# Optimization experiments

Hardware: AMD Instinct MI355X
Metric: run time of the kernel (lower is better)

Reference implementation:

```python
import jax, jax.numpy as jnp
import numpy as np

NUM_HEADS = 16
ROPE_BASE = 10000.0


def _rope(x):
    # x: (B, T, H, D); torchtune-style interleaved rotary embedding
    B, T, H, D = x.shape
    inv_freq = 1.0 / (ROPE_BASE ** (jnp.arange(0, D, 2, dtype=jnp.float32) / D))  # (D/2,)
    ang = jnp.arange(T, dtype=jnp.float32)[:, None] * inv_freq[None, :]  # (T, D/2)
    cos = jnp.cos(ang)[None, :, None, :].astype(x.dtype)  # (1,T,1,D/2)
    sin = jnp.sin(ang)[None, :, None, :].astype(x.dtype)
    x1 = x[..., 0::2]
    x2 = x[..., 1::2]
    r1 = x1 * cos - x2 * sin
    r2 = x2 * cos + x1 * sin
    return jnp.stack([r1, r2], axis=-1).reshape(B, T, H, D)


def _attention(x, Wq, Wk, Wv, Wo, bo):
    B, T, C = x.shape
    H = NUM_HEADS
    D = C // H
    q = (x @ Wq).reshape(B, T, H, D)
    k = (x @ Wk).reshape(B, T, H, D)
    v = (x @ Wv).reshape(B, T, H, D)
    q = _rope(q)
    k = _rope(k)
    # (B, H, T, D)
    q = q.transpose(0, 2, 1, 3)
    k = k.transpose(0, 2, 1, 3)
    v = v.transpose(0, 2, 1, 3)
    scale = 1.0 / jnp.sqrt(jnp.asarray(D, dtype=x.dtype))
    scores = jnp.einsum('bhqd,bhkd->bhqk', q, k) * scale  # (B,H,T,T)
    causal = jnp.tril(jnp.ones((T, T), dtype=bool))
    scores = jnp.where(causal[None, None, :, :], scores, jnp.asarray(-jnp.inf, dtype=scores.dtype))
    attn = jax.nn.softmax(scores, axis=-1)
    out = jnp.einsum('bhqk,bhkd->bhqd', attn, v)  # (B,H,T,D)
    out = out.transpose(0, 2, 1, 3).reshape(B, T, C)
    return out @ Wo + bo  # dropout is identity in eval mode


def setup_inputs() -> dict:
    key = jax.random.key(0)
    ks = jax.random.split(key, 6)
    B, T, C = 2, 2048, 1024
    s = 1.0 / np.sqrt(C)
    return {
        'x': jax.random.normal(ks[0], (B, T, C), dtype=jnp.float32),
        'Wq': jax.random.normal(ks[1], (C, C), dtype=jnp.float32) * s,
        'Wk': jax.random.normal(ks[2], (C, C), dtype=jnp.float32) * s,
        'Wv': jax.random.normal(ks[3], (C, C), dtype=jnp.float32) * s,
        'Wo': jax.random.normal(ks[4], (C, C), dtype=jnp.float32) * s,
        'bo': jnp.zeros((C,), dtype=jnp.float32),
    }


def reference(x, Wq, Wk, Wv, Wo, bo):
    return _attention(x, Wq, Wk, Wv, Wo, bo)
```

## Files before the change

### kernel.cpp

```cpp
#include <hip/hip_runtime.h>
#include <stdint.h>

#define BATCH 2
#define T_SEQ 2048
#define CDIM  1024
#define NH    16
#define HD    64
#define MROWS (BATCH*T_SEQ)

typedef unsigned short u16;
typedef __attribute__((ext_vector_type(8))) short bf16x8;
typedef __attribute__((ext_vector_type(4))) float f32x4;
typedef __attribute__((ext_vector_type(16))) float f32x16;
typedef __attribute__((ext_vector_type(4))) unsigned short u16x4;

__constant__ int qc_tab[40] = {0,1,2,3, 4,4,5,5,6,6,7,7,
                               8,8,8,9,9,9,10,10,10,11,11,11,
                               12,12,12,12,13,13,13,13,14,14,14,14,15,15,15,15};
__constant__ int ck_tab[40] = {0,0,0,0, 0,1,0,1,0,1,0,1,
                               0,1,2,0,1,2,0,1,2,0,1,2,
                               0,1,2,3,0,1,2,3,0,1,2,3,0,1,2,3};
__constant__ int base_tab[16] = {0,1,2,3,4,6,8,10,12,15,18,21,24,28,32,36};
__constant__ int nch_tab[16]  = {1,1,1,1,2,2,2,2,3,3,3,3,4,4,4,4};

__device__ __forceinline__ u16 f2b(float f) {
  union { float f; unsigned int u; } x; x.f = f;
  unsigned int r = x.u + 0x7FFFu + ((x.u >> 16) & 1u);
  return (u16)(r >> 16);
}

__device__ __forceinline__ void gload16(const void* g, void* s) {
  __builtin_amdgcn_global_load_lds(
      (const __attribute__((address_space(1))) void*)g,
      (__attribute__((address_space(3))) void*)s, 16, 0, 0);
}

__device__ __forceinline__ int cvtpk(float lo, float hi_) {
  int w;
  asm("v_cvt_pk_bf16_f32 %0, %1, %2" : "=v"(w) : "v"(lo), "v"(hi_));
  return w;
}

__device__ __forceinline__ bf16x8 mkfrag(int a, int b, int c, int d) {
  union { int i[4]; bf16x8 v; } u;
  u.i[0] = a; u.i[1] = b; u.i[2] = c; u.i[3] = d;
  return u.v;
}

__global__ __launch_bounds__(256) void cvt4(const float4* __restrict__ in,
                                            u16x4* __restrict__ out, int n4) {
  int i = blockIdx.x * 256 + threadIdx.x;
  if (i < n4) {
    float4 v = in[i];
    u16x4 o = { f2b(v.x), f2b(v.y), f2b(v.z), f2b(v.w) };
    out[i] = o;
  }
}

__global__ __launch_bounds__(256) void w_trans4(const float* __restrict__ W0,
                                                const float* __restrict__ W1,
                                                const float* __restrict__ W2,
                                                const float* __restrict__ W3,
                                                u16* __restrict__ D0,
                                                u16* __restrict__ D3) {
  __shared__ u16 tile[64][72];
  const float* W = (blockIdx.z == 0) ? W0 : (blockIdx.z == 1) ? W1
                 : (blockIdx.z == 2) ? W2 : W3;
  u16* Wt = (blockIdx.z == 3) ? D3 : (D0 + (size_t)blockIdx.z * CDIM * CDIM);
  int k0 = blockIdx.x * 64, n0 = blockIdx.y * 64;
  int tid = threadIdx.x;
  #pragma unroll
  for (int i = 0; i < 16; ++i) {
    int c = i * 256 + tid;
    int kr = c >> 6, nc = c & 63;
    tile[kr][nc] = f2b(W[(size_t)(k0 + kr) * CDIM + n0 + nc]);
  }
  __syncthreads();
  #pragma unroll
  for (int i = 0; i < 16; ++i) {
    int c = i * 256 + tid;
    int nr = c >> 6, kc = c & 63;
    Wt[(size_t)(n0 + nr) * CDIM + k0 + kc] = tile[kc][nr];
  }
}

__global__ __launch_bounds__(256) void rope_tab(float* __restrict__ cosT,
                                                float* __restrict__ sinT) {
  int i = blockIdx.x * 256 + threadIdx.x;
  int t = i >> 5, j = i & 31;
  float inv = expf(-(float)j * (9.210340371976184f / 32.0f));
  float ang = (float)t * inv;
  cosT[i] = cosf(ang);
  sinT[i] = sinf(ang);
}

__global__ __launch_bounds__(512, 2) void gemm_qkv256(const u16* __restrict__ A,
                                                      const u16* __restrict__ Bt,
                                                      const float* __restrict__ cosT,
                                                      const float* __restrict__ sinT,
                                                      u16* __restrict__ Qr,
                                                      u16* __restrict__ Kr,
                                                      u16* __restrict__ Vt) {
  __shared__ __align__(16) char smem[114688];
  const int tid = threadIdx.x;
  const int wid = tid >> 6, lane = tid & 63;
  const int wm = wid >> 2, wn = wid & 3;
  const int col = lane & 15, kq = lane >> 4;
  const int xcd = blockIdx.x & 7, bi = blockIdx.x >> 3;
  const int arow0 = (bi & 15) * 256;
  const int bcol0 = (xcd * 2 + (bi >> 4)) * 192;

  auto STAGE = [&](int k0, int bsel) {
    char* dA = smem + bsel * 57344;
    char* dB = dA + 32768;
    #pragma unroll
    for (int i = 0; i < 4; ++i) {
      int idx = i * 512 + tid;
      int r = idx >> 3, p = idx & 7;
      int src = (p ^ (r & 7)) << 3;
      gload16(A + (size_t)(arow0 + r) * CDIM + k0 + src, dA + idx * 16);
    }
    #pragma unroll
    for (int i = 0; i < 3; ++i) {
      int idx = i * 512 + tid;
      int r = idx >> 3, p = idx & 7;
      int src = (p ^ (r & 7)) << 3;
      gload16(Bt + (size_t)(bcol0 + r) * CDIM + k0 + src, dB + idx * 16);
    }
  };

  f32x4 acc[8][3] = {};

  STAGE(0, 0);
  for (int kt = 0; kt < 16; ++kt) {
    if (kt < 15) {
      STAGE((kt + 1) * 64, (kt + 1) & 1);
      asm volatile("s_waitcnt vmcnt(7)" ::: "memory");
    } else {
      asm volatile("s_waitcnt vmcnt(0)" ::: "memory");
    }
    __builtin_amdgcn_s_barrier();

    const char* As_ = smem + (kt & 1) * 57344;
    const char* Bs_ = As_ + 32768;

    bf16x8 bfr[3][2], a0[4][2], a1[4][2];
    #pragma unroll
    for (int n = 0; n < 3; ++n)
      #pragma unroll
      for (int ks = 0; ks < 2; ++ks) {
        int rowb = wn * 48 + n * 16 + col;
        bfr[n][ks] = *(const bf16x8*)(Bs_ + rowb * 128 + (((ks * 4 + kq) ^ (rowb & 7)) << 4));
      }
    #pragma unroll
    for (int m = 0; m < 4; ++m)
      #pragma unroll
      for (int ks = 0; ks < 2; ++ks) {
        int row = wm * 128 + m * 16 + col;
        a0[m][ks] = *(const bf16x8*)(As_ + row * 128 + (((ks * 4 + kq) ^ (row & 7)) << 4));
        int row1 = row + 64;
        a1[m][ks] = *(const bf16x8*)(As_ + row1 * 128 + (((ks * 4 + kq) ^ (row1 & 7)) << 4));
      }

    __builtin_amdgcn_s_setprio(1);
    #pragma unroll
    for (int m = 0; m < 4; ++m)
      #pragma unroll
      for (int n = 0; n < 3; ++n)
        #pragma unroll
        for (int ks = 0; ks < 2; ++ks)
          acc[m][n] = __builtin_amdgcn_mfma_f32_16x16x32_bf16(a0[m][ks], bfr[n][ks],
                                                              acc[m][n], 0, 0, 0);
    #pragma unroll
    for (int m = 0; m < 4; ++m)
      #pragma unroll
      for (int n = 0; n < 3; ++n)
        #pragma unroll
        for (int ks = 0; ks < 2; ++ks)
          acc[4 + m][n] = __builtin_amdgcn_mfma_f32_16x16x32_bf16(a1[m][ks], bfr[n][ks],
                                                                  acc[4 + m][n], 0, 0, 0);
    __builtin_amdgcn_s_setprio(0);
    __builtin_amdgcn_s_barrier();
  }

  #pragma unroll
  for (int im = 0; im < 8; ++im)
    #pragma unroll
    for (int in = 0; in < 3; ++in) {
      int cc = bcol0 + wn * 48 + in * 16 + col;
      int type = cc >> 10;
      int cm = cc & 1023;
      int h = cm >> 6, d = cm & 63;
      int rr0 = arow0 + wm * 128 + im * 16 + kq * 4;
      if (type == 2) {
        int b = rr0 >> 11, t = rr0 & 2047;
        u16x4 v4 = { f2b(acc[im][in][0]), f2b(acc[im][in][1]),
                     f2b(acc[im][in][2]), f2b(acc[im][in][3]) };
        *(u16x4*)(Vt + (((size_t)(b * NH + h)) * 64 + d) * T_SEQ + t) = v4;
      } else {
        int j = d >> 1;
        u16* dst = type ? Kr : Qr;
        #pragma unroll
        for (int i = 0; i < 4; ++i) {
          int rr = rr0 + i;
          int b = rr >> 11, t = rr & 2047;
          float val = acc[im][in][i];
          float pv = __shfl_xor(val, 1, 64);
          float c = cosT[t * 32 + j], s = sinT[t * 32 + j];
          float r = (d & 1) ? (val * c + pv * s) : (val * c - pv * s);
          if (type == 0) r *= 0.18033688011112042f;
          dst[(((size_t)(b * NH + h)) * T_SEQ + t) * 64 + d] = f2b(r);
        }
      }
    }
}

__global__ __launch_bounds__(256, 2) void gemm_bt(const u16* __restrict__ A,
                                                  const u16* __restrict__ Bt,
                                                  float* __restrict__ C,
                                                  const float* __restrict__ bias,
                                                  int K, int ldc) {
  __shared__ __align__(16) char smem[65536];
  const int tid = threadIdx.x;
  const int wid = tid >> 6, lane = tid & 63;
  const int wr = wid >> 1, wc = wid & 1;
  const int col = lane & 15, kq = lane >> 4;
  const int swz = (blockIdx.x & 7) * 32 + (blockIdx.x >> 3);
  const int arow0 = (swz & 31) * 128, bcol0 = (swz >> 5) * 128;
  const int NT = K >> 6;

  auto STAGE = [&](int k0, int bsel) {
    char* dA = smem + bsel * 32768;
    char* dB = dA + 16384;
    #pragma unroll
    for (int i = 0; i < 4; ++i) {
      int idx = i * 256 + tid;
      int r = idx >> 3, p = idx & 7;
      int src = (p ^ (r & 7)) << 3;
      gload16(A  + (size_t)(arow0 + r) * K + k0 + src, dA + idx * 16);
      gload16(Bt + (size_t)(bcol0 + r) * K + k0 + src, dB + idx * 16);
    }
  };

  f32x4 acc[4][4] = {};

  STAGE(0, 0);
  for (int kt = 0; kt < NT; ++kt) {
    if (kt + 1 < NT) {
      STAGE((kt + 1) * 64, (kt + 1) & 1);
      asm volatile("s_waitcnt vmcnt(8)" ::: "memory");
    } else {
      asm volatile("s_waitcnt vmcnt(0)" ::: "memory");
    }
    __builtin_amdgcn_s_barrier();
    const char* As_ = smem + (kt & 1) * 32768;
    const char* Bs_ = As_ + 16384;
    bf16x8 a[4][2], b[4][2];
    #pragma unroll
    for (int m = 0; m < 4; ++m)
      #pragma unroll
      for (int ks = 0; ks < 2; ++ks) {
        int row = wr * 64 + m * 16 + col;
        a[m][ks] = *(const bf16x8*)(As_ + row * 128 + (((ks * 4 + kq) ^ (row & 7)) << 4));
      }
    #pragma unroll
    for (int n = 0; n < 4; ++n)
      #pragma unroll
      for (int ks = 0; ks < 2; ++ks) {
        int rowb = wc * 64 + n * 16 + col;
        b[n][ks] = *(const bf16x8*)(Bs_ + rowb * 128 + (((ks * 4 + kq) ^ (rowb & 7)) << 4));
      }
    __builtin_amdgcn_s_setprio(1);
    #pragma unroll
    for (int m = 0; m < 4; ++m)
      #pragma unroll
      for (int n = 0; n < 4; ++n)
        #pragma unroll
        for (int ks = 0; ks < 2; ++ks)
          acc[m][n] = __builtin_amdgcn_mfma_f32_16x16x32_bf16(a[m][ks], b[n][ks],
                                                              acc[m][n], 0, 0, 0);
    __builtin_amdgcn_s_setprio(0);
    __builtin_amdgcn_s_barrier();
  }

  #pragma unroll
  for (int m = 0; m < 4; ++m)
    #pragma unroll
    for (int n = 0; n < 4; ++n) {
      int cc = bcol0 + wc * 64 + n * 16 + col;
      float bv = bias ? bias[cc] : 0.0f;
      #pragma unroll
      for (int i = 0; i < 4; ++i) {
        int rr = arow0 + wr * 64 + m * 16 + kq * 4 + i;
        C[(size_t)rr * ldc + cc] = acc[m][n][i] + bv;
      }
    }
}

__global__ __launch_bounds__(256, 4) void attn_fwd8(const u16* __restrict__ Q,
                                                    const u16* __restrict__ K,
                                                    const u16* __restrict__ V,
                                                    float* __restrict__ OP,
                                                    float* __restrict__ LP) {
  __shared__ __align__(16) char smem[32768];

  const int bh = blockIdx.x;
  const int w = 39 - blockIdx.y;
  const int qc = qc_tab[w], ck = ck_tab[w];
  const int q0 = qc << 7;
  const int nkt = 2 * (qc + 1);
  const int start = ck * 8;
  const int end = min(start + 8, nkt);
  const int slot = w * 32 + bh;

  const int tid = threadIdx.x;
  const int wid = tid >> 6, lane = tid & 63;
  const int l31 = lane & 31, hi = lane >> 5;
  const int wq0 = q0 + wid * 32;
  const int qrow = wq0 + l31;

  bf16x8 qa[4];
  const u16* qbase = Q + ((size_t)bh * T_SEQ + qrow) * 64 + hi * 8;
  #pragma unroll
  for (int dk = 0; dk < 4; ++dk)
    qa[dk] = *(const bf16x8*)(qbase + dk * 16);

  const u16* kb = K + (size_t)bh * T_SEQ * 64;
  const u16* vb = V + (size_t)bh * 64 * T_SEQ;

  auto STAGE = [&](int kt, int bsel) {
    char* dstK = smem + bsel * 16384;
    char* dstV = dstK + 8192;
    int kv0 = kt << 6;
    #pragma unroll
    for (int i = 0; i < 2; ++i) {
      int idx = i * 256 + tid;
      int r = idx >> 3, c = idx & 7;
      int cs = (c ^ (r & 7)) << 3;
      gload16(kb + (size_t)(kv0 + r) * 64 + cs, dstK + idx * 16);
      gload16(vb + (size_t)r * T_SEQ + kv0 + cs, dstV + idx * 16);
    }
  };

  float L = 0.f;
  f32x16 ot0 = {}, ot1 = {};
  const int swl = (l31 & 7);

  STAGE(start, 0);

  for (int kt = start; kt < end; ++kt) {
    const int kv0 = kt << 6;
    const int cur = (kt - start) & 1;
    if (kt + 1 < end) {
      STAGE(kt + 1, cur ^ 1);
      asm volatile("s_waitcnt vmcnt(4)" ::: "memory");
    } else {
      asm volatile("s_waitcnt vmcnt(0)" ::: "memory");
    }
    __builtin_amdgcn_s_barrier();

    if (kv0 <= wq0 + 31) {
      const char* Ks = smem + cur * 16384;
      const char* Vs = Ks + 8192;

      f32x16 st0 = {}, st1 = {};
      __builtin_amdgcn_s_setprio(1);
      #pragma unroll
      for (int dk = 0; dk < 4; ++dk) {
        int ch = dk * 2 + hi;
        bf16x8 ka0 = *(const bf16x8*)(Ks + l31 * 128 + ((ch ^ swl) << 4));
        bf16x8 ka1 = *(const bf16x8*)(Ks + (l31 + 32) * 128 + ((ch ^ swl) << 4));
        st0 = __builtin_amdgcn_mfma_f32_32x32x16_bf16(ka0, qa[dk], st0, 0, 0, 0);
        st1 = __builtin_amdgcn_mfma_f32_32x32x16_bf16(ka1, qa[dk], st1, 0, 0, 0);
      }
      __builtin_amdgcn_s_setprio(0);

      if (kv0 + 63 > wq0) {
        #pragma unroll
        for (int r = 0; r < 16; ++r) {
          int kl = (r & 3) + 8 * (r >> 2) + 4 * hi;
          if (kv0 + kl > qrow)      st0[r] = -1e30f;
          if (kv0 + 32 + kl > qrow) st1[r] = -1e30f;
        }
      }

      float s0 = 0.f, s1 = 0.f, s2 = 0.f, s3 = 0.f;
      #pragma unroll
      for (int r = 0; r < 16; r += 4) {
        st0[r]     = exp2f(st0[r]     - 14.f); st1[r]     = exp2f(st1[r]     - 14.f);
        st0[r + 1] = exp2f(st0[r + 1] - 14.f); st1[r + 1] = exp2f(st1[r + 1] - 14.f);
        st0[r + 2] = exp2f(st0[r + 2] - 14.f); st1[r + 2] = exp2f(st1[r + 2] - 14.f);
        st0[r + 3] = exp2f(st0[r + 3] - 14.f); st1[r + 3] = exp2f(st1[r + 3] - 14.f);
        s0 += st0[r]     + st1[r];
        s1 += st0[r + 1] + st1[r + 1];
        s2 += st0[r + 2] + st1[r + 2];
        s3 += st0[r + 3] + st1[r + 3];
      }
      float sum = (s0 + s1) + (s2 + s3);
      sum += __shfl_xor(sum, 32, 64);
      L += sum;

      int x0 = cvtpk(st0[0], st0[1]),   y0 = cvtpk(st0[4], st0[5]);
      int x1 = cvtpk(st0[2], st0[3]),   y1 = cvtpk(st0[6], st0[7]);
      int x2 = cvtpk(st0[8], st0[9]),   y2 = cvtpk(st0[12], st0[13]);
      int x3 = cvtpk(st0[10], st0[11]), y3 = cvtpk(st0[14], st0[15]);
      asm("v_permlane32_swap_b32 %0, %1" : "+v"(x0), "+v"(y0));
      asm("v_permlane32_swap_b32 %0, %1" : "+v"(x1), "+v"(y1));
      asm("v_permlane32_swap_b32 %0, %1" : "+v"(x2), "+v"(y2));
      asm("v_permlane32_swap_b32 %0, %1" : "+v"(x3), "+v"(y3));
      int z0 = cvtpk(st1[0], st1[1]),   w0 = cvtpk(st1[4], st1[5]);
      int z1 = cvtpk(st1[2], st1[3]),   w1 = cvtpk(st1[6], st1[7]);
      int z2 = cvtpk(st1[8], st1[9]),   w2 = cvtpk(st1[12], st1[13]);
      int z3 = cvtpk(st1[10], st1[11]), w3 = cvtpk(st1[14], st1[15]);
      asm("v_permlane32_swap_b32 %0, %1" : "+v"(z0), "+v"(w0));
      asm("v_permlane32_swap_b32 %0, %1" : "+v"(z1), "+v"(w1));
      asm("v_permlane32_swap_b32 %0, %1" : "+v"(z2), "+v"(w2));
      asm("v_permlane32_swap_b32 %0, %1" : "+v"(z3), "+v"(w3));
      bf16x8 pb[4];
      pb[0] = mkfrag(x0, x1, y0, y1);
      pb[1] = mkfrag(x2, x3, y2, y3);
      pb[2] = mkfrag(z0, z1, w0, w1);
      pb[3] = mkfrag(z2, z3, w2, w3);

      __builtin_amdgcn_s_setprio(1);
      #pragma unroll
      for (int ks = 0; ks < 4; ++ks) {
        int ch = ks * 2 + hi;
        bf16x8 va0 = *(const bf16x8*)(Vs + l31 * 128 + ((ch ^ swl) << 4));
        bf16x8 va1 = *(const bf16x8*)(Vs + (l31 + 32) * 128 + ((ch ^ swl) << 4));
        ot0 = __builtin_amdgcn_mfma_f32_32x32x16_bf16(va0, pb[ks], ot0, 0, 0, 0);
        ot1 = __builtin_amdgcn_mfma_f32_32x32x16_bf16(va1, pb[ks], ot1, 0, 0, 0);
      }
      __builtin_amdgcn_s_setprio(0);
    }

    asm volatile("s_waitcnt lgkmcnt(0)" ::: "memory");
    __builtin_amdgcn_s_barrier();
  }

  float* op = OP + (size_t)slot * 8192;
  const int qloc = wid * 32 + l31;
  #pragma unroll
  for (int r = 0; r < 16; ++r) {
    int d_ = (r & 3) + 8 * (r >> 2) + 4 * hi;
    op[d_ * 128 + qloc]        = ot0[r];
    op[(32 + d_) * 128 + qloc] = ot1[r];
  }
  if (hi == 0) LP[(size_t)slot * 128 + qloc] = L;
}

__global__ __launch_bounds__(256) void attn_comb(const float* __restrict__ OP,
                                                 const float* __restrict__ LP,
                                                 u16* __restrict__ Ob) {
  __shared__ float tr[64 * 132];
  const int qc = blockIdx.x, head = blockIdx.y;
  const int nch = nch_tab[qc], base = base_tab[qc];
  const int tid = threadIdx.x;

  {
    int d = tid >> 2, q4 = (tid & 3) * 32;
    float a[32];
    #pragma unroll
    for (int j = 0; j < 32; ++j) a[j] = 0.f;
    for (int c = 0; c < nch; ++c) {
      const float* p = OP + ((size_t)((base + c) * 32 + head)) * 8192 + d * 128 + q4;
      #pragma unroll
      for (int j = 0; j < 8; ++j) {
        float4 v = *(const float4*)(p + j * 4);
        a[j * 4]     += v.x; a[j * 4 + 1] += v.y;
        a[j * 4 + 2] += v.z; a[j * 4 + 3] += v.w;
      }
    }
    #pragma unroll
    for (int j = 0; j < 32; ++j) tr[d * 132 + q4 + j] = a[j];
  }
  __syncthreads();

  int q = tid >> 1, d0 = (tid & 1) * 32;
  float Lt = 0.f;
  for (int c = 0; c < nch; ++c)
    Lt += LP[((size_t)((base + c) * 32 + head)) * 128 + q];
  float inv = 1.0f / Lt;

  int outw[16];
  #pragma unroll
  for (int j = 0; j < 16; ++j) {
    float lo  = tr[(d0 + 2 * j) * 132 + q] * inv;
    float hi_ = tr[(d0 + 2 * j + 1) * 132 + q] * inv;
    outw[j] = cvtpk(lo, hi_);
  }
  int b = head >> 4, h = head & 15;
  size_t row = (size_t)(b * T_SEQ + qc * 128 + q);
  int* dst = (int*)(Ob + row * 1024 + h * 64 + d0);
  #pragma unroll
  for (int j = 0; j < 4; ++j) {
    int4 v = { outw[j * 4], outw[j * 4 + 1], outw[j * 4 + 2], outw[j * 4 + 3] };
    *(int4*)(dst + j * 4) = v;
  }
}

extern "C" void kernel_launch(void* const* d_in, const int* in_sizes, int n_in,
                              void* d_out, int out_size, void* d_ws, size_t ws_size,
                              hipStream_t stream) {
  (void)in_sizes; (void)n_in; (void)out_size; (void)ws_size;
  const float* x  = (const float*)d_in[0];
  const float* Wq = (const float*)d_in[1];
  const float* Wk = (const float*)d_in[2];
  const float* Wv = (const float*)d_in[3];
  const float* Wo = (const float*)d_in[4];
  const float* bo = (const float*)d_in[5];
  float* out = (float*)d_out;

  char* ws = (char*)d_ws;
  u16*   xb   = (u16*)(ws);
  u16*   Wqkv = (u16*)(ws + (size_t)( 8u << 20));
  u16*   Wot  = (u16*)(ws + (size_t)(14u << 20));
  u16*   Qr   = (u16*)(ws + (size_t)(16u << 20));
  u16*   Kr   = (u16*)(ws + (size_t)(24u << 20));
  u16*   Vt   = (u16*)(ws + (size_t)(32u << 20));
  u16*   Ob   = (u16*)(ws + (size_t)(40u << 20));
  float* cosT = (float*)(ws + (size_t)(48u << 20));
  float* sinT = (float*)(ws + (size_t)(48u << 20) + (1u << 18));
  float* OP   = (float*)(ws + (size_t)(49u << 20));
  float* LP   = (float*)(ws + (size_t)(89u << 20));

  cvt4<<<dim3(MROWS * CDIM / 4 / 256), dim3(256), 0, stream>>>(
      (const float4*)x, (u16x4*)xb, MROWS * CDIM / 4);
  w_trans4<<<dim3(16, 16, 4), dim3(256), 0, stream>>>(Wq, Wk, Wv, Wo, Wqkv, Wot);
  rope_tab<<<dim3(T_SEQ * 32 / 256), dim3(256), 0, stream>>>(cosT, sinT);

  gemm_qkv256<<<dim3(256), dim3(512), 0, stream>>>(xb, Wqkv, cosT, sinT, Qr, Kr, Vt);

  attn_fwd8<<<dim3(32, 40), dim3(256), 0, stream>>>(Qr, Kr, Vt, OP, LP);
  attn_comb<<<dim3(16, 32), dim3(256), 0, stream>>>(OP, LP, Ob);

  gemm_bt<<<dim3(256), dim3(256), 0, stream>>>(Ob, Wot, out, bo, CDIM, CDIM);
}
```

Before: 116.4 us.

## Give each attention wave two 32-row query tiles, halving block size

The flash-attention kernel now runs 2 waves per block instead of 4, and each wave handles 64 query rows as two 32-row sub-tiles that share the same K and V fragments loaded from LDS. Staging loops are widened so 128 threads still fill the same K/V tiles, and the wait counts are adjusted to match. The aim is to cut LDS reads per MFMA and barrier overhead. The cost is more VGPRs (twice the accumulators) and lower occupancy, plus coarser causal skipping per wave.

```diff
diff --git a/kernel.cpp b/kernel.cpp
--- a/kernel.cpp
+++ b/kernel.cpp
@@ -297,7 +297,7 @@
     }
 }
 
-__global__ __launch_bounds__(256, 4) void attn_fwd8(const u16* __restrict__ Q,
+__global__ __launch_bounds__(128, 2) void attn_fwd9(const u16* __restrict__ Q,
                                                     const u16* __restrict__ K,
                                                     const u16* __restrict__ V,
                                                     float* __restrict__ OP,
@@ -316,14 +316,17 @@
   const int tid = threadIdx.x;
   const int wid = tid >> 6, lane = tid & 63;
   const int l31 = lane & 31, hi = lane >> 5;
-  const int wq0 = q0 + wid * 32;
-  const int qrow = wq0 + l31;
-
-  bf16x8 qa[4];
-  const u16* qbase = Q + ((size_t)bh * T_SEQ + qrow) * 64 + hi * 8;
-  #pragma unroll
-  for (int dk = 0; dk < 4; ++dk)
-    qa[dk] = *(const bf16x8*)(qbase + dk * 16);
+  const int wq0 = q0 + wid * 64;
+  const int qrowA = wq0 + l31;
+  const int qrowB = wq0 + 32 + l31;
+
+  bf16x8 qaA[4], qaB[4];
+  const u16* qbA = Q + ((size_t)bh * T_SEQ + qrowA) * 64 + hi * 8;
+  #pragma unroll
+  for (int dk = 0; dk < 4; ++dk) {
+    qaA[dk] = *(const bf16x8*)(qbA + dk * 16);
+    qaB[dk] = *(const bf16x8*)(qbA + 2048 + dk * 16);
+  }
 
   const u16* kb = K + (size_t)bh * T_SEQ * 64;
   const u16* vb = V + (size_t)bh * 64 * T_SEQ;
@@ -333,8 +336,8 @@
     char* dstV = dstK + 8192;
     int kv0 = kt << 6;
     #pragma unroll
-    for (int i = 0; i < 2; ++i) {
-      int idx = i * 256 + tid;
+    for (int i = 0; i < 4; ++i) {
+      int idx = i * 128 + tid;
       int r = idx >> 3, c = idx & 7;
       int cs = (c ^ (r & 7)) << 3;
       gload16(kb + (size_t)(kv0 + r) * 64 + cs, dstK + idx * 16);
@@ -342,8 +345,8 @@
     }
   };
 
-  float L = 0.f;
-  f32x16 ot0 = {}, ot1 = {};
+  float LA = 0.f, LB = 0.f;
+  f32x16 oA0 = {}, oA1 = {}, oB0 = {}, oB1 = {};
   const int swl = (l31 & 7);
 
   STAGE(start, 0);
@@ -353,25 +356,27 @@
     const int cur = (kt - start) & 1;
     if (kt + 1 < end) {
       STAGE(kt + 1, cur ^ 1);
-      asm volatile("s_waitcnt vmcnt(4)" ::: "memory");
+      asm volatile("s_waitcnt vmcnt(8)" ::: "memory");
     } else {
       asm volatile("s_waitcnt vmcnt(0)" ::: "memory");
     }
     __builtin_amdgcn_s_barrier();
 
-    if (kv0 <= wq0 + 31) {
+    if (kv0 <= wq0 + 63) {
       const char* Ks = smem + cur * 16384;
       const char* Vs = Ks + 8192;
 
-      f32x16 st0 = {}, st1 = {};
+      f32x16 sA0 = {}, sA1 = {}, sB0 = {}, sB1 = {};
       __builtin_amdgcn_s_setprio(1);
       #pragma unroll
       for (int dk = 0; dk < 4; ++dk) {
         int ch = dk * 2 + hi;
         bf16x8 ka0 = *(const bf16x8*)(Ks + l31 * 128 + ((ch ^ swl) << 4));
         bf16x8 ka1 = *(const bf16x8*)(Ks + (l31 + 32) * 128 + ((ch ^ swl) << 4));
-        st0 = __builtin_amdgcn_mfma_f32_32x32x16_bf16(ka0, qa[dk], st0, 0, 0, 0);
-        st1 = __builtin_amdgcn_mfma_f32_32x32x16_bf16(ka1, qa[dk], st1, 0, 0, 0);
+        sA0 = __builtin_amdgcn_mfma_f32_32x32x16_bf16(ka0, qaA[dk], sA0, 0, 0, 0);
+        sA1 = __builtin_amdgcn_mfma_f32_32x32x16_bf16(ka1, qaA[dk], sA1, 0, 0, 0);
+        sB0 = __builtin_amdgcn_mfma_f32_32x32x16_bf16(ka0, qaB[dk], sB0, 0, 0, 0);
+        sB1 = __builtin_amdgcn_mfma_f32_32x32x16_bf16(ka1, qaB[dk], sB1, 0, 0, 0);
       }
       __builtin_amdgcn_s_setprio(0);
 
@@ -379,48 +384,78 @@
         #pragma unroll
         for (int r = 0; r < 16; ++r) {
           int kl = (r & 3) + 8 * (r >> 2) + 4 * hi;
-          if (kv0 + kl > qrow)      st0[r] = -1e30f;
-          if (kv0 + 32 + kl > qrow) st1[r] = -1e30f;
+          if (kv0 + kl > qrowA)      sA0[r] = -1e30f;
+          if (kv0 + 32 + kl > qrowA) sA1[r] = -1e30f;
         }
       }
-
-      float s0 = 0.f, s1 = 0.f, s2 = 0.f, s3 = 0.f;
-      #pragma unroll
-      for (int r = 0; r < 16; r += 4) {
-        st0[r]     = exp2f(st0[r]     - 14.f); st1[r]     = exp2f(st1[r]     - 14.f);
-        st0[r + 1] = exp2f(st0[r + 1] - 14.f); st1[r + 1] = exp2f(st1[r + 1] - 14.f);
-        st0[r + 2] = exp2f(st0[r + 2] - 14.f); st1[r + 2] = exp2f(st1[r + 2] - 14.f);
-        st0[r + 3] = exp2f(st0[r + 3] - 14.f); st1[r + 3] = exp2f(st1[r + 3] - 14.f);
-        s0 += st0[r]     + st1[r];
-        s1 += st0[r + 1] + st1[r + 1];
-        s2 += st0[r + 2] + st1[r + 2];
-        s3 += st0[r + 3] + st1[r + 3];
-      }
-      float sum = (s0 + s1) + (s2 + s3);
-      sum += __shfl_xor(sum, 32, 64);
-      L += sum;
-
-      int x0 = cvtpk(st0[0], st0[1]),   y0 = cvtpk(st0[4], st0[5]);
-      int x1 = cvtpk(st0[2], st0[3]),   y1 = cvtpk(st0[6], st0[7]);
-      int x2 = cvtpk(st0[8], st0[9]),   y2 = cvtpk(st0[12], st0[13]);
-      int x3 = cvtpk(st0[10], st0[11]), y3 = cvtpk(st0[14], st0[15]);
+      if (kv0 + 63 > wq0 + 32) {
+        #pragma unroll
+        for (int r = 0; r < 16; ++r) {
+          int kl = (r & 3) + 8 * (r >> 2) + 4 * hi;
+          if (kv0 + kl > qrowB)      sB0[r] = -1e30f;
+          if (kv0 + 32 + kl > qrowB) sB1[r] = -1e30f;
+        }
+      }
+
+      float a0_ = 0.f, a1_ = 0.f, b0_ = 0.f, b1_ = 0.f;
+      #pragma unroll
+      for (int r = 0; r < 16; r += 2) {
+        sA0[r]     = exp2f(sA0[r]     - 14.f); sA1[r]     = exp2f(sA1[r]     - 14.f);
+        sA0[r + 1] = exp2f(sA0[r + 1] - 14.f); sA1[r + 1] = exp2f(sA1[r + 1] - 14.f);
+        sB0[r]     = exp2f(sB0[r]     - 14.f); sB1[r]     = exp2f(sB1[r]     - 14.f);
+        sB0[r + 1] = exp2f(sB0[r + 1] - 14.f); sB1[r + 1] = exp2f(sB1[r + 1] - 14.f);
+        a0_ += sA0[r] + sA1[r];  a1_ += sA0[r + 1] + sA1[r + 1];
+        b0_ += sB0[r] + sB1[r];  b1_ += sB0[r + 1] + sB1[r + 1];
+      }
+      float sa = a0_ + a1_, sb = b0_ + b1_;
+      sa += __shfl_xor(sa, 32, 64);
+      sb += __shfl_xor(sb, 32, 64);
+      LA += sa;
+      LB += sb;
+
+      int x0 = cvtpk(sA0[0], sA0[1]),   y0 = cvtpk(sA0[4], sA0[5]);
+      int x1 = cvtpk(sA0[2], sA0[3]),   y1 = cvtpk(sA0[6], sA0[7]);
+      int x2 = cvtpk(sA0[8], sA0[9]),   y2 = cvtpk(sA0[12], sA0[13]);
+      int x3 = cvtpk(sA0[10], sA0[11]), y3 = cvtpk(sA0[14], sA0[15]);
       asm("v_permlane32_swap_b32 %0, %1" : "+v"(x0), "+v"(y0));
       asm("v_permlane32_swap_b32 %0, %1" : "+v"(x1), "+v"(y1));
       asm("v_permlane32_swap_b32 %0, %1" : "+v"(x2), "+v"(y2));
       asm("v_permlane32_swap_b32 %0, %1" : "+v"(x3), "+v"(y3));
-      int z0 = cvtpk(st1[0], st1[1]),   w0 = cvtpk(st1[4], st1[5]);
-      int z1 = cvtpk(st1[2], st1[3]),   w1 = cvtpk(st1[6], st1[7]);
-      int z2 = cvtpk(st1[8], st1[9]),   w2 = cvtpk(st1[12], st1[13]);
-      int z3 = cvtpk(st1[10], st1[11]), w3 = cvtpk(st1[14], st1[15]);
+      int z0 = cvtpk(sA1[0], sA1[1]),   w0 = cvtpk(sA1[4], sA1[5]);
+      int z1 = cvtpk(sA1[2], sA1[3]),   w1 = cvtpk(sA1[6], sA1[7]);
+      int z2 = cvtpk(sA1[8], sA1[9]),   w2 = cvtpk(sA1[12], sA1[13]);
+      int z3 = cvtpk(sA1[10], sA1[11]), w3 = cvtpk(sA1[14], sA1[15]);
       asm("v_permlane32_swap_b32 %0, %1" : "+v"(z0), "+v"(w0));
       asm("v_permlane32_swap_b32 %0, %1" : "+v"(z1), "+v"(w1));
       asm("v_permlane32_swap_b32 %0, %1" : "+v"(z2), "+v"(w2));
       asm("v_permlane32_swap_b32 %0, %1" : "+v"(z3), "+v"(w3));
-      bf16x8 pb[4];
-      pb[0] = mkfrag(x0, x1, y0, y1);
-      pb[1] = mkfrag(x2, x3, y2, y3);
-      pb[2] = mkfrag(z0, z1, w0, w1);
-      pb[3] = mkfrag(z2, z3, w2, w3);
+      bf16x8 pbA[4];
+      pbA[0] = mkfrag(x0, x1, y0, y1);
+      pbA[1] = mkfrag(x2, x3, y2, y3);
+      pbA[2] = mkfrag(z0, z1, w0, w1);
+      pbA[3] = mkfrag(z2, z3, w2, w3);
+
+      x0 = cvtpk(sB0[0], sB0[1]);   y0 = cvtpk(sB0[4], sB0[5]);
+      x1 = cvtpk(sB0[2], sB0[3]);   y1 = cvtpk(sB0[6], sB0[7]);
+      x2 = cvtpk(sB0[8], sB0[9]);   y2 = cvtpk(sB0[12], sB0[13]);
+      x3 = cvtpk(sB0[10], sB0[11]); y3 = cvtpk(sB0[14], sB0[15]);
+      asm("v_permlane32_swap_b32 %0, %1" : "+v"(x0), "+v"(y0));
+      asm("v_permlane32_swap_b32 %0, %1" : "+v"(x1), "+v"(y1));
+      asm("v_permlane32_swap_b32 %0, %1" : "+v"(x2), "+v"(y2));
+      asm("v_permlane32_swap_b32 %0, %1" : "+v"(x3), "+v"(y3));
+      z0 = cvtpk(sB1[0], sB1[1]);   w0 = cvtpk(sB1[4], sB1[5]);
+      z1 = cvtpk(sB1[2], sB1[3]);   w1 = cvtpk(sB1[6], sB1[7]);
+      z2 = cvtpk(sB1[8], sB1[9]);   w2 = cvtpk(sB1[12], sB1[13]);
+      z3 = cvtpk(sB1[10], sB1[11]); w3 = cvtpk(sB1[14], sB1[15]);
+      asm("v_permlane32_swap_b32 %0, %1" : "+v"(z0), "+v"(w0));
+      asm("v_permlane32_swap_b32 %0, %1" : "+v"(z1), "+v"(w1));
+      asm("v_permlane32_swap_b32 %0, %1" : "+v"(z2), "+v"(w2));
+      asm("v_permlane32_swap_b32 %0, %1" : "+v"(z3), "+v"(w3));
+      bf16x8 pbB[4];
+      pbB[0] = mkfrag(x0, x1, y0, y1);
+      pbB[1] = mkfrag(x2, x3, y2, y3);
+      pbB[2] = mkfrag(z0, z1, w0, w1);
+      pbB[3] = mkfrag(z2, z3, w2, w3);
 
       __builtin_amdgcn_s_setprio(1);
       #pragma unroll
@@ -428,8 +463,10 @@
         int ch = ks * 2 + hi;
         bf16x8 va0 = *(const bf16x8*)(Vs + l31 * 128 + ((ch ^ swl) << 4));
         bf16x8 va1 = *(const bf16x8*)(Vs + (l31 + 32) * 128 + ((ch ^ swl) << 4));
-        ot0 = __builtin_amdgcn_mfma_f32_32x32x16_bf16(va0, pb[ks], ot0, 0, 0, 0);
-        ot1 = __builtin_amdgcn_mfma_f32_32x32x16_bf16(va1, pb[ks], ot1, 0, 0, 0);
+        oA0 = __builtin_amdgcn_mfma_f32_32x32x16_bf16(va0, pbA[ks], oA0, 0, 0, 0);
+        oA1 = __builtin_amdgcn_mfma_f32_32x32x16_bf16(va1, pbA[ks], oA1, 0, 0, 0);
+        oB0 = __builtin_amdgcn_mfma_f32_32x32x16_bf16(va0, pbB[ks], oB0, 0, 0, 0);
+        oB1 = __builtin_amdgcn_mfma_f32_32x32x16_bf16(va1, pbB[ks], oB1, 0, 0, 0);
       }
       __builtin_amdgcn_s_setprio(0);
     }
@@ -439,14 +476,19 @@
   }
 
   float* op = OP + (size_t)slot * 8192;
-  const int qloc = wid * 32 + l31;
+  const int qA = wid * 64 + l31, qB = qA + 32;
   #pragma unroll
   for (int r = 0; r < 16; ++r) {
     int d_ = (r & 3) + 8 * (r >> 2) + 4 * hi;
-    op[d_ * 128 + qloc]        = ot0[r];
-    op[(32 + d_) * 128 + qloc] = ot1[r];
-  }
-  if (hi == 0) LP[(size_t)slot * 128 + qloc] = L;
+    op[d_ * 128 + qA]        = oA0[r];
+    op[(32 + d_) * 128 + qA] = oA1[r];
+    op[d_ * 128 + qB]        = oB0[r];
+    op[(32 + d_) * 128 + qB] = oB1[r];
+  }
+  if (hi == 0) {
+    LP[(size_t)slot * 128 + qA] = LA;
+    LP[(size_t)slot * 128 + qB] = LB;
+  }
 }
 
 __global__ __launch_bounds__(256) void attn_comb(const float* __restrict__ OP,
@@ -531,7 +573,7 @@
 
   gemm_qkv256<<<dim3(256), dim3(512), 0, stream>>>(xb, Wqkv, cosT, sinT, Qr, Kr, Vt);
 
-  attn_fwd8<<<dim3(32, 40), dim3(256), 0, stream>>>(Qr, Kr, Vt, OP, LP);
+  attn_fwd9<<<dim3(32, 40), dim3(128), 0, stream>>>(Qr, Kr, Vt, OP, LP);
   attn_comb<<<dim3(16, 32), dim3(256), 0, stream>>>(OP, LP, Ob);
 
   gemm_bt<<<dim3(256), dim3(256), 0, stream>>>(Ob, Wot, out, bo, CDIM, CDIM);
```

Measured after the change: 129.0 us. 1.11x slower.
